# Kernel optimization log

Hardware: AMD Instinct MI355X
Metric: run time of the kernel (lower is better)

## Reference

```python
import jax, jax.numpy as jnp
import numpy as np

EMBED = 768
HEADS = 12
HEAD_DIM = EMBED // HEADS


def setup_inputs() -> dict:
    key = jax.random.key(0)
    ks = jax.random.split(key, 9)
    B, S, E = 2, 2048, EMBED
    sc = 1.0 / np.sqrt(E)
    return {
        "x": jax.random.normal(ks[0], (B, S, E), dtype=jnp.float32),
        "Wq": jax.random.normal(ks[1], (E, E), dtype=jnp.float32) * sc,
        "bq": jnp.zeros((E,), dtype=jnp.float32),
        "Wk": jax.random.normal(ks[2], (E, E), dtype=jnp.float32) * sc,
        "bk": jnp.zeros((E,), dtype=jnp.float32),
        "Wv": jax.random.normal(ks[3], (E, E), dtype=jnp.float32) * sc,
        "bv": jnp.zeros((E,), dtype=jnp.float32),
        "Wo": jax.random.normal(ks[4], (E, E), dtype=jnp.float32) * sc,
        "bo": jnp.zeros((E,), dtype=jnp.float32),
    }


def _split_heads(t):
    B, S, E = t.shape
    return t.reshape(B, S, HEADS, HEAD_DIM).transpose(0, 2, 1, 3)  # [B,H,S,D]


def reference(x, Wq, bq, Wk, bk, Wv, bv, Wo, bo):
    B, S, E = x.shape
    Q = _split_heads(x @ Wq + bq)
    K = _split_heads(x @ Wk + bk)
    V = _split_heads(x @ Wv + bv)
    scale = 1.0 / jnp.sqrt(jnp.asarray(HEAD_DIM, dtype=x.dtype))
    scores = jnp.einsum("bhqd,bhkd->bhqk", Q, K) * scale  # [B,H,S,S]
    attn_weights = jax.nn.softmax(scores, axis=-1)
    attn = jnp.einsum("bhqk,bhkd->bhqd", attn_weights, V)  # [B,H,S,D]
    attn = attn.transpose(0, 2, 1, 3).reshape(B, S, E)
    out = attn @ Wo + bo
    return out, attn_weights
```

## Files before the change

### kernel.cpp

```cpp
#include <hip/hip_runtime.h>
#include <cstddef>

#define B_ 2
#define S_ 2048
#define E_ 768
#define H_ 12
#define D_ 64
#define M_ (B_*S_)

typedef float f4 __attribute__((ext_vector_type(4)));
typedef short short8 __attribute__((ext_vector_type(8)));

__device__ __forceinline__ short f2bf(float f) {
    union { float f; unsigned u; } v; v.f = f;
    unsigned r = (v.u + 0x7fffu + ((v.u >> 16) & 1u)) >> 16;
    return (short)r;
}

__global__ __launch_bounds__(256) void cvt_bf16_k(const float* __restrict__ in,
                                                  short* __restrict__ out, int n8)
{
    int i = blockIdx.x * 256 + threadIdx.x;
    if (i >= n8) return;
    f4 a = *(const f4*)(in + (size_t)i * 8);
    f4 b = *(const f4*)(in + (size_t)i * 8 + 4);
    short8 o;
    o[0] = f2bf(a[0]); o[1] = f2bf(a[1]); o[2] = f2bf(a[2]); o[3] = f2bf(a[3]);
    o[4] = f2bf(b[0]); o[5] = f2bf(b[1]); o[6] = f2bf(b[2]); o[7] = f2bf(b[3]);
    *(short8*)(out + (size_t)i * 8) = o;
}

__global__ __launch_bounds__(256) void wtrans_k(const float* __restrict__ Wq,
                                                const float* __restrict__ Wk,
                                                const float* __restrict__ Wv,
                                                const float* __restrict__ Wo,
                                                short* __restrict__ Wt)
{
    __shared__ float T[32][33];
    const float* W = (blockIdx.z == 0) ? Wq : (blockIdx.z == 1) ? Wk
                   : (blockIdx.z == 2) ? Wv : Wo;
    short* o = Wt + (size_t)blockIdx.z * E_ * E_;
    const int tx = threadIdx.x & 31, ty = threadIdx.x >> 5;
    const int k0 = blockIdx.y * 32, n0 = blockIdx.x * 32;
    #pragma unroll
    for (int i = 0; i < 4; ++i)
        T[ty * 4 + i][tx] = W[(size_t)(k0 + ty * 4 + i) * E_ + n0 + tx];
    __syncthreads();
    #pragma unroll
    for (int i = 0; i < 4; ++i)
        o[(size_t)(n0 + ty * 4 + i) * E_ + k0 + tx] = f2bf(T[tx][ty * 4 + i]);
}

template<int MODE>
__global__ __launch_bounds__(256) void gemm_mfma_k(
    const short* __restrict__ A, const short* __restrict__ Bt,
    const float* __restrict__ bias, float* __restrict__ outf,
    short* __restrict__ outb, float scale)
{
    __shared__ short8 As[64][8];
    __shared__ short8 Bs[64][8];
    const int t = threadIdx.x;
    const int w = t >> 6, lane = t & 63, ln = lane & 15, quad = lane >> 4;
    const int m0 = blockIdx.y * 64, n0 = blockIdx.x * 64;

    f4 acc[4];
    #pragma unroll
    for (int i = 0; i < 4; ++i) acc[i] = (f4){0.f, 0.f, 0.f, 0.f};

    for (int k0 = 0; k0 < E_; k0 += 64) {
        __syncthreads();
        #pragma unroll
        for (int i = 0; i < 2; ++i) {
            int c = t + i * 256, r = c >> 3, cc = c & 7;
            As[r][cc ^ (r & 7)] =
                *(const short8*)(A  + (size_t)(m0 + r) * E_ + k0 + cc * 8);
            Bs[r][cc ^ (r & 7)] =
                *(const short8*)(Bt + (size_t)(n0 + r) * E_ + k0 + cc * 8);
        }
        __syncthreads();
        const int ar = w * 16 + ln;
        short8 af0 = As[ar][quad ^ (ar & 7)];
        short8 af1 = As[ar][(quad + 4) ^ (ar & 7)];
        #pragma unroll
        for (int ng = 0; ng < 4; ++ng) {
            int br = ng * 16 + ln;
            short8 bf0 = Bs[br][quad ^ (br & 7)];
            short8 bf1 = Bs[br][(quad + 4) ^ (br & 7)];
            acc[ng] = __builtin_amdgcn_mfma_f32_16x16x32_bf16(af0, bf0, acc[ng], 0, 0, 0);
            acc[ng] = __builtin_amdgcn_mfma_f32_16x16x32_bf16(af1, bf1, acc[ng], 0, 0, 0);
        }
    }

    #pragma unroll
    for (int ng = 0; ng < 4; ++ng) {
        int c = n0 + ng * 16 + ln;
        float bv = bias[c];
        #pragma unroll
        for (int g = 0; g < 4; ++g) {
            int r = m0 + w * 16 + quad * 4 + g;
            float v = acc[ng][g] + bv;
            if (MODE == 0) {
                outf[(size_t)r * E_ + c] = v;
            } else {
                int b = r >> 11, s = r & (S_ - 1);
                int h = c >> 6,  d = c & (D_ - 1);
                if (MODE == 1)
                    outb[((size_t)(b * H_ + h) * S_ + s) * D_ + d] = f2bf(v * scale);
                else
                    outb[((size_t)(b * H_ + h) * D_ + d) * S_ + s] = f2bf(v);
            }
        }
    }
}

__global__ __launch_bounds__(256) void attn_k(
    const short* __restrict__ Qb, const short* __restrict__ Kb,
    const short* __restrict__ Vt, float* __restrict__ P,
    short* __restrict__ ctxb)
{
    __shared__ short8 KT[64][8];
    __shared__ short8 VT[64][8];
    __shared__ short  PT[4][16][72];

    const int t    = threadIdx.x;
    const int w    = t >> 6;
    const int lane = t & 63, ln = lane & 15, quad = lane >> 4;
    const int bh   = blockIdx.y;
    const int qr   = blockIdx.x * 64 + w * 16;

    const size_t kvbase = (size_t)bh * S_ * D_;

    short8 qf0, qf1;
    {
        const short* qrow = Qb + kvbase + (size_t)(qr + ln) * D_;
        qf0 = *(const short8*)(qrow + quad * 8);
        qf1 = *(const short8*)(qrow + 32 + quad * 8);
    }

    f4 l_acc = {0.f, 0.f, 0.f, 0.f};

    for (int k0 = 0; k0 < S_; k0 += 64) {
        __syncthreads();
        #pragma unroll
        for (int i = 0; i < 2; ++i) {
            int c = t + i * 256, r = c >> 3, cc = c & 7;
            KT[r][cc ^ (r & 7)] =
                *(const short8*)(Kb + kvbase + (size_t)(k0 + r) * D_ + cc * 8);
        }
        __syncthreads();
        #pragma unroll
        for (int kg = 0; kg < 4; ++kg) {
            int row = kg * 16 + ln;
            short8 kf0 = KT[row][quad ^ (row & 7)];
            short8 kf1 = KT[row][(quad + 4) ^ (row & 7)];
            f4 sc = {0.f, 0.f, 0.f, 0.f};
            sc = __builtin_amdgcn_mfma_f32_16x16x32_bf16(qf0, kf0, sc, 0, 0, 0);
            sc = __builtin_amdgcn_mfma_f32_16x16x32_bf16(qf1, kf1, sc, 0, 0, 0);
            #pragma unroll
            for (int g = 0; g < 4; ++g) l_acc[g] += __expf(sc[g] - 8.0f);
        }
    }

    f4 inv_l;
    #pragma unroll
    for (int g = 0; g < 4; ++g) {
        float v = l_acc[g];
        v += __shfl_xor(v, 1, 64);
        v += __shfl_xor(v, 2, 64);
        v += __shfl_xor(v, 4, 64);
        v += __shfl_xor(v, 8, 64);
        inv_l[g] = 1.0f / v;
    }

    f4 acc[4];
    #pragma unroll
    for (int dg = 0; dg < 4; ++dg) acc[dg] = (f4){0.f, 0.f, 0.f, 0.f};

    float* Pw = P + ((size_t)bh * S_ + qr) * S_;

    for (int k0 = 0; k0 < S_; k0 += 64) {
        __syncthreads();
        #pragma unroll
        for (int i = 0; i < 2; ++i) {
            int c = t + i * 256, r = c >> 3, cc = c & 7;
            KT[r][cc ^ (r & 7)] =
                *(const short8*)(Kb + kvbase + (size_t)(k0 + r) * D_ + cc * 8);
            VT[r][cc ^ (r & 7)] =
                *(const short8*)(Vt + kvbase + (size_t)r * S_ + k0 + cc * 8);
        }
        __syncthreads();
        #pragma unroll
        for (int kg = 0; kg < 4; ++kg) {
            int row = kg * 16 + ln;
            short8 kf0 = KT[row][quad ^ (row & 7)];
            short8 kf1 = KT[row][(quad + 4) ^ (row & 7)];
            f4 sc = {0.f, 0.f, 0.f, 0.f};
            sc = __builtin_amdgcn_mfma_f32_16x16x32_bf16(qf0, kf0, sc, 0, 0, 0);
            sc = __builtin_amdgcn_mfma_f32_16x16x32_bf16(qf1, kf1, sc, 0, 0, 0);
            #pragma unroll
            for (int g = 0; g < 4; ++g) {
                float p = __expf(sc[g] - 8.0f) * inv_l[g];
                Pw[(size_t)(quad * 4 + g) * S_ + k0 + kg * 16 + ln] = p;
                PT[w][quad * 4 + g][kg * 16 + ln] = f2bf(p);
            }
        }
        __syncthreads();
        short8 af0 = *(const short8*)&PT[w][ln][quad * 8];
        short8 af1 = *(const short8*)&PT[w][ln][32 + quad * 8];
        #pragma unroll
        for (int dg = 0; dg < 4; ++dg) {
            int row = dg * 16 + ln;
            short8 vf0 = VT[row][quad ^ (row & 7)];
            short8 vf1 = VT[row][(quad + 4) ^ (row & 7)];
            acc[dg] = __builtin_amdgcn_mfma_f32_16x16x32_bf16(af0, vf0, acc[dg], 0, 0, 0);
            acc[dg] = __builtin_amdgcn_mfma_f32_16x16x32_bf16(af1, vf1, acc[dg], 0, 0, 0);
        }
    }

    const int b = bh / H_, h = bh % H_;
    #pragma unroll
    for (int dg = 0; dg < 4; ++dg)
        #pragma unroll
        for (int g = 0; g < 4; ++g)
            ctxb[(size_t)(b * S_ + qr + quad * 4 + g) * E_ + h * D_ + dg * 16 + ln]
                = f2bf(acc[dg][g]);
}

extern "C" void kernel_launch(void* const* d_in, const int* in_sizes, int n_in,
                              void* d_out, int out_size, void* d_ws, size_t ws_size,
                              hipStream_t stream) {
    const float* x  = (const float*)d_in[0];
    const float* Wq = (const float*)d_in[1];
    const float* bq = (const float*)d_in[2];
    const float* Wk = (const float*)d_in[3];
    const float* bk = (const float*)d_in[4];
    const float* Wv = (const float*)d_in[5];
    const float* bv = (const float*)d_in[6];
    const float* Wo = (const float*)d_in[7];
    const float* bo = (const float*)d_in[8];

    const size_t NE = (size_t)M_ * E_;
    const size_t W2 = (size_t)E_ * E_;
    short* xb  = (short*)d_ws;
    short* Wt  = xb + NE;
    short* Qb  = Wt + 4 * W2;
    short* Kb  = Qb + NE;
    short* Vtb = Kb + NE;
    short* Cb  = Vtb + NE;

    float* out0  = (float*)d_out;
    float* attnw = out0 + NE;

    cvt_bf16_k<<<dim3((int)(NE / 8 / 256)), 256, 0, stream>>>(x, xb, (int)(NE / 8));
    wtrans_k<<<dim3(24, 24, 4), 256, 0, stream>>>(Wq, Wk, Wv, Wo, Wt);

    dim3 gg(E_ / 64, M_ / 64);
    gemm_mfma_k<1><<<gg, 256, 0, stream>>>(xb, Wt + 0 * W2, bq, nullptr, Qb, 0.125f);
    gemm_mfma_k<1><<<gg, 256, 0, stream>>>(xb, Wt + 1 * W2, bk, nullptr, Kb, 1.0f);
    gemm_mfma_k<2><<<gg, 256, 0, stream>>>(xb, Wt + 2 * W2, bv, nullptr, Vtb, 1.0f);
    attn_k<<<dim3(S_ / 64, B_ * H_), 256, 0, stream>>>(Qb, Kb, Vtb, attnw, Cb);
    gemm_mfma_k<0><<<gg, 256, 0, stream>>>(Cb, Wt + 3 * W2, bo, out0, nullptr, 1.0f);
}
```

Baseline: 548.0 us.

## Double-buffer LDS tiles with async global_load_lds prefetch in GEMM and attention

Replaces register-staged global-to-LDS copies with direct global_load_lds transfers into double-buffered LDS tiles. The next K/V (or A/B) tile is issued before computing on the current one, and each loop iteration needs one barrier instead of two. This aims to hide global load latency behind MFMA work, at the cost of doubled LDS use and reliance on barrier waitcnt ordering for async LDS writes.

```diff
diff --git a/kernel.cpp b/kernel.cpp
--- a/kernel.cpp
+++ b/kernel.cpp
@@ -15,6 +15,22 @@
     union { float f; unsigned u; } v; v.f = f;
     unsigned r = (v.u + 0x7fffu + ((v.u >> 16) & 1u)) >> 16;
     return (short)r;
+}
+
+__device__ __forceinline__ void stage64(const short* __restrict__ g0, int rstride,
+                                        short8* lds, int w, int lane)
+{
+    #pragma unroll
+    for (int i = 0; i < 2; ++i) {
+        const int n = w * 128 + i * 64 + lane;
+        const int r = n >> 3, s = n & 7;
+        const int cc = s ^ (r & 7);
+        const short* src = g0 + (size_t)r * rstride + cc * 8;
+        __builtin_amdgcn_global_load_lds(
+            (const __attribute__((address_space(1))) unsigned int*)src,
+            (__attribute__((address_space(3))) unsigned int*)(lds + w * 128 + i * 64),
+            16, 0, 0);
+    }
 }
 
 __global__ __launch_bounds__(256) void cvt_bf16_k(const float* __restrict__ in,
@@ -57,38 +73,42 @@
     const float* __restrict__ bias, float* __restrict__ outf,
     short* __restrict__ outb, float scale)
 {
-    __shared__ short8 As[64][8];
-    __shared__ short8 Bs[64][8];
+    __shared__ short8 As[2][64][8];
+    __shared__ short8 Bs[2][64][8];
     const int t = threadIdx.x;
     const int w = t >> 6, lane = t & 63, ln = lane & 15, quad = lane >> 4;
     const int m0 = blockIdx.y * 64, n0 = blockIdx.x * 64;
 
+    const short* Ab = A  + (size_t)m0 * E_;
+    const short* Bb = Bt + (size_t)n0 * E_;
+
     f4 acc[4];
     #pragma unroll
     for (int i = 0; i < 4; ++i) acc[i] = (f4){0.f, 0.f, 0.f, 0.f};
 
+    stage64(Ab, E_, &As[0][0][0], w, lane);
+    stage64(Bb, E_, &Bs[0][0][0], w, lane);
+    __syncthreads();
+
+    int cb = 0;
     for (int k0 = 0; k0 < E_; k0 += 64) {
-        __syncthreads();
-        #pragma unroll
-        for (int i = 0; i < 2; ++i) {
-            int c = t + i * 256, r = c >> 3, cc = c & 7;
-            As[r][cc ^ (r & 7)] =
-                *(const short8*)(A  + (size_t)(m0 + r) * E_ + k0 + cc * 8);
-            Bs[r][cc ^ (r & 7)] =
-                *(const short8*)(Bt + (size_t)(n0 + r) * E_ + k0 + cc * 8);
-        }
-        __syncthreads();
+        if (k0 + 64 < E_) {
+            stage64(Ab + k0 + 64, E_, &As[cb ^ 1][0][0], w, lane);
+            stage64(Bb + k0 + 64, E_, &Bs[cb ^ 1][0][0], w, lane);
+        }
         const int ar = w * 16 + ln;
-        short8 af0 = As[ar][quad ^ (ar & 7)];
-        short8 af1 = As[ar][(quad + 4) ^ (ar & 7)];
+        short8 af0 = As[cb][ar][quad ^ (ar & 7)];
+        short8 af1 = As[cb][ar][(quad + 4) ^ (ar & 7)];
         #pragma unroll
         for (int ng = 0; ng < 4; ++ng) {
             int br = ng * 16 + ln;
-            short8 bf0 = Bs[br][quad ^ (br & 7)];
-            short8 bf1 = Bs[br][(quad + 4) ^ (br & 7)];
+            short8 bf0 = Bs[cb][br][quad ^ (br & 7)];
+            short8 bf1 = Bs[cb][br][(quad + 4) ^ (br & 7)];
             acc[ng] = __builtin_amdgcn_mfma_f32_16x16x32_bf16(af0, bf0, acc[ng], 0, 0, 0);
             acc[ng] = __builtin_amdgcn_mfma_f32_16x16x32_bf16(af1, bf1, acc[ng], 0, 0, 0);
         }
+        __syncthreads();
+        cb ^= 1;
     }
 
     #pragma unroll
@@ -118,8 +138,8 @@
     const short* __restrict__ Vt, float* __restrict__ P,
     short* __restrict__ ctxb)
 {
-    __shared__ short8 KT[64][8];
-    __shared__ short8 VT[64][8];
+    __shared__ short8 KT[2][64][8];
+    __shared__ short8 VT[2][64][8];
     __shared__ short  PT[4][16][72];
 
     const int t    = threadIdx.x;
@@ -129,6 +149,8 @@
     const int qr   = blockIdx.x * 64 + w * 16;
 
     const size_t kvbase = (size_t)bh * S_ * D_;
+    const short* Kbase = Kb + kvbase;
+    const short* Vbase = Vt + kvbase;
 
     short8 qf0, qf1;
     {
@@ -139,26 +161,25 @@
 
     f4 l_acc = {0.f, 0.f, 0.f, 0.f};
 
+    stage64(Kbase, D_, &KT[0][0][0], w, lane);
+    __syncthreads();
+    int cb = 0;
     for (int k0 = 0; k0 < S_; k0 += 64) {
-        __syncthreads();
-        #pragma unroll
-        for (int i = 0; i < 2; ++i) {
-            int c = t + i * 256, r = c >> 3, cc = c & 7;
-            KT[r][cc ^ (r & 7)] =
-                *(const short8*)(Kb + kvbase + (size_t)(k0 + r) * D_ + cc * 8);
-        }
-        __syncthreads();
+        if (k0 + 64 < S_)
+            stage64(Kbase + (size_t)(k0 + 64) * D_, D_, &KT[cb ^ 1][0][0], w, lane);
         #pragma unroll
         for (int kg = 0; kg < 4; ++kg) {
             int row = kg * 16 + ln;
-            short8 kf0 = KT[row][quad ^ (row & 7)];
-            short8 kf1 = KT[row][(quad + 4) ^ (row & 7)];
+            short8 kf0 = KT[cb][row][quad ^ (row & 7)];
+            short8 kf1 = KT[cb][row][(quad + 4) ^ (row & 7)];
             f4 sc = {0.f, 0.f, 0.f, 0.f};
             sc = __builtin_amdgcn_mfma_f32_16x16x32_bf16(qf0, kf0, sc, 0, 0, 0);
             sc = __builtin_amdgcn_mfma_f32_16x16x32_bf16(qf1, kf1, sc, 0, 0, 0);
             #pragma unroll
             for (int g = 0; g < 4; ++g) l_acc[g] += __expf(sc[g] - 8.0f);
         }
+        __syncthreads();
+        cb ^= 1;
     }
 
     f4 inv_l;
@@ -178,22 +199,20 @@
 
     float* Pw = P + ((size_t)bh * S_ + qr) * S_;
 
+    stage64(Kbase, D_, &KT[0][0][0], w, lane);
+    stage64(Vbase, S_, &VT[0][0][0], w, lane);
+    __syncthreads();
+    cb = 0;
     for (int k0 = 0; k0 < S_; k0 += 64) {
-        __syncthreads();
-        #pragma unroll
-        for (int i = 0; i < 2; ++i) {
-            int c = t + i * 256, r = c >> 3, cc = c & 7;
-            KT[r][cc ^ (r & 7)] =
-                *(const short8*)(Kb + kvbase + (size_t)(k0 + r) * D_ + cc * 8);
-            VT[r][cc ^ (r & 7)] =
-                *(const short8*)(Vt + kvbase + (size_t)r * S_ + k0 + cc * 8);
-        }
-        __syncthreads();
+        if (k0 + 64 < S_) {
+            stage64(Kbase + (size_t)(k0 + 64) * D_, D_, &KT[cb ^ 1][0][0], w, lane);
+            stage64(Vbase + k0 + 64,                S_, &VT[cb ^ 1][0][0], w, lane);
+        }
         #pragma unroll
         for (int kg = 0; kg < 4; ++kg) {
             int row = kg * 16 + ln;
-            short8 kf0 = KT[row][quad ^ (row & 7)];
-            short8 kf1 = KT[row][(quad + 4) ^ (row & 7)];
+            short8 kf0 = KT[cb][row][quad ^ (row & 7)];
+            short8 kf1 = KT[cb][row][(quad + 4) ^ (row & 7)];
             f4 sc = {0.f, 0.f, 0.f, 0.f};
             sc = __builtin_amdgcn_mfma_f32_16x16x32_bf16(qf0, kf0, sc, 0, 0, 0);
             sc = __builtin_amdgcn_mfma_f32_16x16x32_bf16(qf1, kf1, sc, 0, 0, 0);
@@ -204,17 +223,18 @@
                 PT[w][quad * 4 + g][kg * 16 + ln] = f2bf(p);
             }
         }
-        __syncthreads();
         short8 af0 = *(const short8*)&PT[w][ln][quad * 8];
         short8 af1 = *(const short8*)&PT[w][ln][32 + quad * 8];
         #pragma unroll
         for (int dg = 0; dg < 4; ++dg) {
             int row = dg * 16 + ln;
-            short8 vf0 = VT[row][quad ^ (row & 7)];
-            short8 vf1 = VT[row][(quad + 4) ^ (row & 7)];
+            short8 vf0 = VT[cb][row][quad ^ (row & 7)];
+            short8 vf1 = VT[cb][row][(quad + 4) ^ (row & 7)];
             acc[dg] = __builtin_amdgcn_mfma_f32_16x16x32_bf16(af0, vf0, acc[dg], 0, 0, 0);
             acc[dg] = __builtin_amdgcn_mfma_f32_16x16x32_bf16(af1, vf1, acc[dg], 0, 0, 0);
         }
+        __syncthreads();
+        cb ^= 1;
     }
 
     const int b = bh / H_, h = bh % H_;
```

After: 563.3 us. 1.03x slower.
